# Optimization experiments

Measured on AMD Instinct MI355X. Metric: run time of the kernel, lower is better.

The kernel has to match this reference:

```python
import jax, jax.numpy as jnp
import numpy as np

H = 32        # query heads
KVH = 8       # key/value heads
D = 64        # head_dim
HID = 2048
B, S = 2, 2048

def rotate_half(x):
    x1, x2 = x[..., :D // 2], x[..., D // 2:]
    return jnp.concatenate((-x2, x1), axis=-1)

def setup_inputs() -> dict:
    key = jax.random.key(0)
    ks = jax.random.split(key, 7)
    scale = 1.0 / np.sqrt(HID)
    return {
        "x": jax.random.normal(ks[0], (B, S, HID), jnp.float32),
        "cos": jax.random.uniform(ks[1], (S, D), jnp.float32),
        "sin": jax.random.uniform(ks[2], (S, D), jnp.float32),
        "wq": jax.random.normal(ks[3], (HID, H * D), jnp.float32) * scale,
        "wk": jax.random.normal(ks[4], (HID, KVH * D), jnp.float32) * scale,
        "wv": jax.random.normal(ks[5], (HID, KVH * D), jnp.float32) * scale,
        "wo": jax.random.normal(ks[6], (HID, HID), jnp.float32) * scale,
    }

def reference(x, cos, sin, wq, wk, wv, wo):
    b, s, _ = x.shape
    # QKV projections -> [b, heads, s, d]
    q = (x @ wq).reshape(b, s, H, D).transpose(0, 2, 1, 3)
    k = (x @ wk).reshape(b, s, KVH, D).transpose(0, 2, 1, 3)
    v = (x @ wv).reshape(b, s, KVH, D).transpose(0, 2, 1, 3)
    # RoPE (cos/sin broadcast over batch and heads)
    c = cos[None, None, :, :]
    si = sin[None, None, :, :]
    q = q * c + rotate_half(q) * si
    k = k * c + rotate_half(k) * si
    # GQA: expand kv heads (repeat_interleave on head axis)
    g = H // KVH
    k = jnp.repeat(k, g, axis=1)
    v = jnp.repeat(v, g, axis=1)
    # causal SDPA
    scores = jnp.einsum("bhqd,bhkd->bhqk", q, k) / np.sqrt(D).astype(np.float32)
    causal = jnp.tril(jnp.ones((s, s), dtype=bool))
    scores = jnp.where(causal[None, None], scores, jnp.finfo(scores.dtype).min)
    attn = jax.nn.softmax(scores, axis=-1)
    out = jnp.einsum("bhqk,bhkd->bhqd", attn, v)
    out = out.transpose(0, 2, 1, 3).reshape(b, s, H * D)
    return out @ wo
```

## Files before the change

kernel.cpp:

```cpp
#include <hip/hip_runtime.h>
#include <stdint.h>

#define B_ 2
#define S_ 2048
#define H_ 32
#define KVH_ 8
#define D_ 64
#define HID_ 2048

typedef float f32x4 __attribute__((ext_vector_type(4)));
typedef float f32x16 __attribute__((ext_vector_type(16)));
typedef short bf16x8 __attribute__((ext_vector_type(8)));
typedef unsigned short u16;
typedef unsigned short u16x4 __attribute__((ext_vector_type(4)));
typedef unsigned short u16x8 __attribute__((ext_vector_type(8)));
typedef unsigned int u32;
typedef unsigned int u32x2 __attribute__((ext_vector_type(2)));
typedef unsigned int u32x4 __attribute__((ext_vector_type(4)));

__device__ __forceinline__ u16 f2b(float f) {
  unsigned u = __builtin_bit_cast(unsigned, f);
  u += 0x7fffu + ((u >> 16) & 1u);
  return (u16)(u >> 16);
}
__device__ __forceinline__ float b2f(u16 h) {
  unsigned u = ((unsigned)h) << 16;
  return __builtin_bit_cast(float, u);
}
__device__ __forceinline__ void gl_lds16(const void* g, void* l) {
  __builtin_amdgcn_global_load_lds(
      (const __attribute__((address_space(1))) unsigned*)g,
      (__attribute__((address_space(3))) unsigned*)l, 16, 0, 0);
}
__device__ __forceinline__ f32x4 mfma16(bf16x8 a, bf16x8 b, f32x4 c) {
  return __builtin_amdgcn_mfma_f32_16x16x32_bf16(a, b, c, 0, 0, 0);
}
__device__ __forceinline__ f32x16 mfma32(bf16x8 a, bf16x8 b, f32x16 c) {
  return __builtin_amdgcn_mfma_f32_32x32x16_bf16(a, b, c, 0, 0, 0);
}
__device__ __forceinline__ u32 cvtpk(float lo, float hi) {
  u32 r;
  asm("v_cvt_pk_bf16_f32 %0, %1, %2" : "=v"(r) : "v"(lo), "v"(hi));
  return r;
}
__device__ __forceinline__ float fast_exp2(float x) {
#if __has_builtin(__builtin_amdgcn_exp2f)
  return __builtin_amdgcn_exp2f(x);
#else
  return exp2f(x);
#endif
}
__device__ __forceinline__ void swap32(u32 a, u32 b, u32& x, u32& y) {
#if __has_builtin(__builtin_amdgcn_permlane32_swap)
  auto r = __builtin_amdgcn_permlane32_swap(a, b, false, false);
  x = r[0];
  y = r[1];
#else
  u32 sa = (u32)__shfl_xor((int)a, 32), sb = (u32)__shfl_xor((int)b, 32);
  bool hib = (threadIdx.x & 32) != 0;
  x = hib ? sb : a;
  y = hib ? b : sa;
#endif
}

__global__ __launch_bounds__(256) void k_prep(const float* __restrict__ x,
                                              u16* __restrict__ xb,
                                              const float* __restrict__ wq,
                                              const float* __restrict__ wk,
                                              const float* __restrict__ wv,
                                              const float* __restrict__ wo,
                                              u16* __restrict__ wqkvT,
                                              u16* __restrict__ woT) {
  __shared__ float t[32][33];
  int bx = blockIdx.x;
  if (bx < 8192) {
    int i = bx * 256 + threadIdx.x;
    f32x4 v = *(const f32x4*)(x + (size_t)i * 4);
    u16x4 o;
    o[0] = f2b(v[0]); o[1] = f2b(v[1]); o[2] = f2b(v[2]); o[3] = f2b(v[3]);
    *(u16x4*)(xb + (size_t)i * 4) = o;
    return;
  }
  int tt2 = bx - 8192;
  int bxx = tt2 % 160;
  int ky = tt2 / 160;
  const int K = 2048;
  const float* src;
  u16* dst;
  int N, n0;
  if (bxx < 64) {
    src = wq; dst = wqkvT; N = 2048; n0 = bxx * 32;
  } else if (bxx < 80) {
    src = wk; dst = wqkvT + (size_t)2048 * 2048; N = 512; n0 = (bxx - 64) * 32;
  } else if (bxx < 96) {
    src = wv; dst = wqkvT + (size_t)2560 * 2048; N = 512; n0 = (bxx - 80) * 32;
  } else {
    src = wo; dst = woT; N = 2048; n0 = (bxx - 96) * 32;
  }
  int k0 = ky * 32;
  int tt = threadIdx.x;
  int r = tt >> 3, c4 = (tt & 7) << 2;
  f32x4 v = *(const f32x4*)(src + (size_t)(k0 + r) * N + n0 + c4);
  t[r][c4 + 0] = v[0]; t[r][c4 + 1] = v[1];
  t[r][c4 + 2] = v[2]; t[r][c4 + 3] = v[3];
  __syncthreads();
  u16x4 o;
  o[0] = f2b(t[c4 + 0][r]); o[1] = f2b(t[c4 + 1][r]);
  o[2] = f2b(t[c4 + 2][r]); o[3] = f2b(t[c4 + 3][r]);
  *(u16x4*)(dst + (size_t)(n0 + r) * K + k0 + c4) = o;
}

__device__ __forceinline__ void stage64(const u16* __restrict__ G, int rowbase,
                                        int K, int kt, u16* unit, int tid) {
  int r = tid >> 3, sl = tid & 7;
  gl_lds16(G + (size_t)(rowbase + r) * K + kt * 64 + ((sl ^ (r & 7)) << 3),
           (char*)unit + tid * 16);
}

template <int BN, int OUTF32>
__global__ __launch_bounds__(512, 1) void k_gemm8(const u16* __restrict__ A,
                                                  const u16* __restrict__ BT,
                                                  float* __restrict__ Cf,
                                                  u16* __restrict__ Cb,
                                                  int M, int N, int K) {
  constexpr int ATILE = 256 * 64;
  constexpr int BTILE = BN * 64;
  constexpr int BU = BN / 64;
  constexpr int WN = (BN == 128) ? 2 : 4;
  constexpr int NI = (BN == 192) ? 3 : 4;
  constexpr int MI = (BN == 128) ? 4 : 8;
  constexpr int MIP = MI / 4;
  __shared__ __align__(16) u16 sm[2 * ATILE + 2 * BTILE];
  const int tid = threadIdx.x;
  const int l = tid & 63;
  const int lg = (l >> 4) & 3, lr = l & 15;
  const int w = tid >> 6;
  const int wm = w / WN, wn = w % WN;

  const int nwg = gridDim.x;
  const int cpx = nwg >> 3;
  const int bid = blockIdx.x;
  const int swz = (bid & 7) * cpx + (bid >> 3);
  const int ntn = N / BN;
  const int bm = swz / ntn, bn = swz % ntn;
  const int m0 = bm << 8, n0 = bn * BN;

  const u16* Ag = A + (size_t)m0 * K;
  const u16* Bg = BT + (size_t)n0 * K;
  u16* As = sm;
  u16* Bs = sm + 2 * ATILE;

  const int nt = K >> 6;
  f32x4 acc[MI][NI] = {};

#pragma unroll
  for (int u = 0; u < 4; ++u) stage64(Ag, u * 64, K, 0, As + u * 4096, tid);
#pragma unroll
  for (int u = 0; u < BU; ++u) stage64(Bg, u * 64, K, 0, Bs + u * 4096, tid);
  stage64(Ag, 0, K, 1, As + ATILE, tid);
  stage64(Ag, 64, K, 1, As + ATILE + 4096, tid);
  asm volatile("s_waitcnt vmcnt(2)" ::: "memory");
  __builtin_amdgcn_s_barrier();
  asm volatile("" ::: "memory");

  for (int t = 0; t < nt; ++t) {
    const int cur = t & 1;
    u16* Ac = As + cur * ATILE;
    u16* Bc = Bs + cur * BTILE;
    u16* An = As + (cur ^ 1) * ATILE;
    u16* Bn = Bs + (cur ^ 1) * BTILE;
    bf16x8 bc[NI][2];
#pragma unroll
    for (int q = 0; q < 4; ++q) {
      bf16x8 af[MIP][2];
#pragma unroll
      for (int mi2 = 0; mi2 < MIP; ++mi2)
#pragma unroll
        for (int ks = 0; ks < 2; ++ks) {
          int row = wm * (MI * 16) + (q * MIP + mi2) * 16 + lr;
          int slot = (ks * 4 + lg) ^ (lr & 7);
          af[mi2][ks] = *(const bf16x8*)&Ac[row * 64 + slot * 8];
        }
      if (q == 0) {
#pragma unroll
        for (int ni = 0; ni < NI; ++ni)
#pragma unroll
          for (int ks = 0; ks < 2; ++ks) {
            int row = wn * (NI * 16) + ni * 16 + lr;
            int slot = (ks * 4 + lg) ^ (lr & 7);
            bc[ni][ks] = *(const bf16x8*)&Bc[row * 64 + slot * 8];
          }
      }
      if (t + 1 < nt) {
        if (q == 0) {
          stage64(Ag, 128, K, t + 1, An + 2 * 4096, tid);
          stage64(Ag, 192, K, t + 1, An + 3 * 4096, tid);
        } else if (q == 1) {
          stage64(Bg, 0, K, t + 1, Bn, tid);
          stage64(Bg, 64, K, t + 1, Bn + 4096, tid);
        } else if (q == 2) {
          if (BU >= 3) stage64(Bg, 128, K, t + 1, Bn + 2 * 4096, tid);
          if (BU >= 4) stage64(Bg, 192, K, t + 1, Bn + 3 * 4096, tid);
        }
      }
      __builtin_amdgcn_s_barrier();
      asm volatile("" ::: "memory");
      __builtin_amdgcn_s_setprio(1);
#pragma unroll
      for (int mi2 = 0; mi2 < MIP; ++mi2)
#pragma unroll
        for (int ni = 0; ni < NI; ++ni)
#pragma unroll
          for (int ks = 0; ks < 2; ++ks)
            acc[q * MIP + mi2][ni] =
                mfma16(af[mi2][ks], bc[ni][ks], acc[q * MIP + mi2][ni]);
      __builtin_amdgcn_s_setprio(0);
      if (q == 3) {
        if (t + 2 < nt) {
          stage64(Ag, 0, K, t + 2, Ac, tid);
          stage64(Ag, 64, K, t + 2, Ac + 4096, tid);
          asm volatile("s_waitcnt vmcnt(2)" ::: "memory");
        } else if (t + 1 < nt) {
          asm volatile("s_waitcnt vmcnt(0)" ::: "memory");
        }
      }
      __builtin_amdgcn_s_barrier();
      asm volatile("" ::: "memory");
    }
  }

#pragma unroll
  for (int mi = 0; mi < MI; ++mi)
#pragma unroll
    for (int ni = 0; ni < NI; ++ni)
#pragma unroll
      for (int j = 0; j < 4; ++j) {
        size_t row = (size_t)m0 + wm * (MI * 16) + mi * 16 + lg * 4 + j;
        size_t col = (size_t)n0 + wn * (NI * 16) + ni * 16 + lr;
        if (OUTF32)
          Cf[row * N + col] = acc[mi][ni][j];
        else
          Cb[row * N + col] = f2b(acc[mi][ni][j]);
      }
}

__global__ __launch_bounds__(256) void k_ropev(const u16* __restrict__ qkv,
                                               const float* __restrict__ cosb,
                                               const float* __restrict__ sinb,
                                               u16* __restrict__ Kr,
                                               u16* __restrict__ Vt) {
  __shared__ u16 t[64][72];
  int bx = blockIdx.x;
  if (bx < 2048) {
    int task = bx * 16 + (threadIdx.x >> 4);
    int t16 = threadIdx.x & 15;
    int kvh = task & 7;
    int row = task >> 3;
    int b = row >> 11, s = row & (S_ - 1);
    int d2 = t16 * 2;
    const u16* base = qkv + (size_t)row * 3072 + 2048 + kvh * 64;
    u32 lo = *(const u32*)(base + d2);
    u32 hi = *(const u32*)(base + d2 + 32);
    float xl0 = b2f((u16)lo), xl1 = b2f((u16)(lo >> 16));
    float xh0 = b2f((u16)hi), xh1 = b2f((u16)(hi >> 16));
    const float* cb = cosb + s * 64;
    const float* sb = sinb + s * 64;
    float cl0 = cb[d2], cl1 = cb[d2 + 1], ch0 = cb[d2 + 32], ch1 = cb[d2 + 33];
    float sl0 = sb[d2], sl1 = sb[d2 + 1], sh0 = sb[d2 + 32], sh1 = sb[d2 + 33];
    float ol0 = xl0 * cl0 - xh0 * sl0;
    float ol1 = xl1 * cl1 - xh1 * sl1;
    float oh0 = xh0 * ch0 + xl0 * sh0;
    float oh1 = xh1 * ch1 + xl1 * sh1;
    u16* dst = Kr + ((size_t)(b * KVH_ + kvh) * S_ + s) * 64;
    *(u32*)(dst + d2) = (u32)f2b(ol0) | ((u32)f2b(ol1) << 16);
    *(u32*)(dst + d2 + 32) = (u32)f2b(oh0) | ((u32)f2b(oh1) << 16);
    return;
  }
  int bid = bx - 2048;
  int st = bid & 31, kvh = (bid >> 5) & 7, b = bid >> 8;
  int s0 = st * 64;
  int tid = threadIdx.x;
  int sl = tid >> 2, c16 = (tid & 3) << 4;
  const u16* src = qkv + (size_t)(b * S_ + s0 + sl) * 3072 + 2560 + kvh * 64 + c16;
  u16x8 v0 = *(const u16x8*)src;
  u16x8 v1 = *(const u16x8*)(src + 8);
#pragma unroll
  for (int i = 0; i < 8; ++i) { t[sl][c16 + i] = v0[i]; t[sl][c16 + 8 + i] = v1[i]; }
  __syncthreads();
  int dl = tid >> 2, s16 = (tid & 3) << 4;
  u16x8 o0, o1;
#pragma unroll
  for (int i = 0; i < 8; ++i) { o0[i] = t[s16 + i][dl]; o1[i] = t[s16 + 8 + i][dl]; }
  u16* dst = Vt + ((size_t)(b * KVH_ + kvh) * 64 + dl) * S_ + s0 + s16;
  *(u16x8*)dst = o0;
  *(u16x8*)(dst + 8) = o1;
}

__device__ __forceinline__ void stage_kv8(const u16* __restrict__ Kg,
                                          const u16* __restrict__ Vg, int k0,
                                          u16* ldsK, u16* ldsV, int tid) {
  int r = tid >> 3, cc = tid & 7;
  gl_lds16(Kg + (size_t)(k0 + r) * 64 + ((cc ^ (r & 7)) << 3), ldsK + tid * 8);
  gl_lds16(Vg + (size_t)r * S_ + k0 + ((cc ^ (r & 7)) << 3), ldsV + tid * 8);
}

__device__ __forceinline__ void repack2(const f32x16 s, bf16x8& f0, bf16x8& f1) {
  bf16x8 outv[2];
#pragma unroll
  for (int h = 0; h < 2; ++h) {
    u32 a0 = cvtpk(s[8 * h + 0], s[8 * h + 1]);
    u32 a1 = cvtpk(s[8 * h + 4], s[8 * h + 5]);
    u32 b0 = cvtpk(s[8 * h + 2], s[8 * h + 3]);
    u32 b1 = cvtpk(s[8 * h + 6], s[8 * h + 7]);
    u32 x0, y0, x1, y1;
    swap32(a0, a1, x0, y0);
    swap32(b0, b1, x1, y1);
    u32x4 t;
    t[0] = x0; t[1] = x1; t[2] = y0; t[3] = y1;
    outv[h] = __builtin_bit_cast(bf16x8, t);
  }
  f0 = outv[0];
  f1 = outv[1];
}

__global__ __launch_bounds__(512) void k_attn(const u16* __restrict__ qkv,
                                              const u16* __restrict__ Kr,
                                              const u16* __restrict__ Vt,
                                              const float* __restrict__ cosb,
                                              const float* __restrict__ sinb,
                                              u16* __restrict__ Oout) {
  __shared__ __align__(16) u16 lds[16384];
  const int tid = threadIdx.x;
  const int w = tid >> 6, l = tid & 63;
  const int hi = l >> 5, l31 = l & 31;

  const int bid = blockIdx.x;
  const int g = bid >> 6;
  const int qtl = (g < 4) ? (7 - g) : (g - 4);
  const int hh = (bid >> 1) & 31;
  const int b = bid & 1;
  const int kvh = hh >> 2;
  const int q0 = qtl * 256;
  const int qw0 = q0 + w * 32;
  const int nt = 4 * qtl + 4;

  int off8[4];
#pragma unroll
  for (int c = 0; c < 4; ++c)
    off8[c] = l31 * 64 + ((((c << 1) | hi) ^ (l31 & 7)) << 3);

  const int s_q = qw0 + l31;
  const u16* qsrc = qkv + (size_t)(b * S_ + s_q) * 3072 + hh * 64;
  bf16x8 qf[4];
  {
    const float* cb = cosb + s_q * 64;
    const float* sb = sinb + s_q * 64;
#pragma unroll
    for (int cp = 0; cp < 2; ++cp) {
      bf16x8 rlo = *(const bf16x8*)(qsrc + cp * 16 + hi * 8);
      bf16x8 rhi = *(const bf16x8*)(qsrc + 32 + cp * 16 + hi * 8);
      int dlo = cp * 16 + hi * 8;
      float ol[8], oh[8];
#pragma unroll
      for (int j = 0; j < 8; ++j) {
        float ql = b2f((u16)rlo[j]), qh = b2f((u16)rhi[j]);
        ol[j] = (ql * cb[dlo + j] - qh * sb[dlo + j]) * 0.18033688f;
        oh[j] = (qh * cb[dlo + 32 + j] + ql * sb[dlo + 32 + j]) * 0.18033688f;
      }
      u32x4 plo, phi;
#pragma unroll
      for (int j2 = 0; j2 < 4; ++j2) {
        plo[j2] = cvtpk(ol[2 * j2], ol[2 * j2 + 1]);
        phi[j2] = cvtpk(oh[2 * j2], oh[2 * j2 + 1]);
      }
      qf[cp] = __builtin_bit_cast(bf16x8, plo);
      qf[cp + 2] = __builtin_bit_cast(bf16x8, phi);
    }
  }

  const u16* Kg = Kr + (size_t)(b * KVH_ + kvh) * S_ * 64;
  const u16* Vg = Vt + (size_t)(b * KVH_ + kvh) * 64 * S_;

  f32x16 o0 = {}, o1 = {};
  float l_run = 0.f;

  stage_kv8(Kg, Vg, 0, lds, lds + 4096, tid);
  asm volatile("s_waitcnt vmcnt(0)" ::: "memory");
  __builtin_amdgcn_s_barrier();
  asm volatile("" ::: "memory");

  for (int kt = 0; kt < nt; ++kt) {
    const int cur = kt & 1;
    const int k0 = kt * 64;
    if (kt + 1 < nt)
      stage_kv8(Kg, Vg, k0 + 64, lds + (cur ^ 1) * 8192,
                lds + (cur ^ 1) * 8192 + 4096, tid);

    if (k0 <= qw0 + 31) {
      const u16* Kc = lds + cur * 8192;
      const u16* Vc = Kc + 4096;

      f32x16 sl = {}, sh = {};
      __builtin_amdgcn_s_setprio(1);
#pragma unroll
      for (int c = 0; c < 4; ++c) {
        bf16x8 klo = *(const bf16x8*)(Kc + off8[c]);
        bf16x8 khi = *(const bf16x8*)(Kc + 2048 + off8[c]);
        sl = mfma32(klo, qf[c], sl);
        sh = mfma32(khi, qf[c], sh);
      }
      __builtin_amdgcn_s_setprio(0);

      if (k0 + 63 > qw0) {
        int qg = qw0 + l31;
#pragma unroll
        for (int r = 0; r < 16; ++r) {
          int kg = k0 + (r & 3) + 8 * (r >> 2) + 4 * hi;
          if (kg > qg) sl[r] = -3e38f;
          if (kg + 32 > qg) sh[r] = -3e38f;
        }
      }

      float smv[16];
#pragma unroll
      for (int i = 0; i < 16; ++i) {
        sl[i] = fast_exp2(sl[i]);
        sh[i] = fast_exp2(sh[i]);
        smv[i] = sl[i] + sh[i];
      }
#pragma unroll
      for (int i = 0; i < 8; ++i) smv[i] += smv[i + 8];
#pragma unroll
      for (int i = 0; i < 4; ++i) smv[i] += smv[i + 4];
      smv[0] = (smv[0] + smv[2]) + (smv[1] + smv[3]);
      l_run += smv[0] + __shfl_xor(smv[0], 32);

      bf16x8 pf[4];
      repack2(sl, pf[0], pf[1]);
      repack2(sh, pf[2], pf[3]);

      __builtin_amdgcn_s_setprio(1);
#pragma unroll
      for (int sub = 0; sub < 4; ++sub) {
        bf16x8 v0 = *(const bf16x8*)(Vc + off8[sub]);
        bf16x8 v1 = *(const bf16x8*)(Vc + 2048 + off8[sub]);
        o0 = mfma32(v0, pf[sub], o0);
        o1 = mfma32(v1, pf[sub], o1);
      }
      __builtin_amdgcn_s_setprio(0);
    }

    asm volatile("s_waitcnt vmcnt(0)" ::: "memory");
    __builtin_amdgcn_s_barrier();
    asm volatile("" ::: "memory");
  }

  {
    u16* ep = lds + w * 2048;
    float inv = 1.0f / l_run;
    float oc[32];
#pragma unroll
    for (int i = 0; i < 16; ++i) { oc[i] = o0[i]; oc[16 + i] = o1[i]; }
#pragma unroll
    for (int dh = 0; dh < 2; ++dh)
#pragma unroll
      for (int g2 = 0; g2 < 4; ++g2) {
        u32 w0 = cvtpk(oc[dh * 16 + 4 * g2 + 0] * inv, oc[dh * 16 + 4 * g2 + 1] * inv);
        u32 w1 = cvtpk(oc[dh * 16 + 4 * g2 + 2] * inv, oc[dh * 16 + 4 * g2 + 3] * inv);
        int col = dh * 32 + 8 * g2 + 4 * hi;
        u32x2 tw; tw[0] = w0; tw[1] = w1;
        *(u32x2*)&ep[l31 * 64 + col] = tw;
      }
    asm volatile("s_waitcnt lgkmcnt(0)" ::: "memory");
    int row = l >> 1;
    size_t gb = ((size_t)(b * S_ + q0 + w * 32 + row)) * HID_ + hh * 64 + (l & 1) * 32;
#pragma unroll
    for (int cc = 0; cc < 4; ++cc) {
      u16x8 v = *(const u16x8*)&ep[row * 64 + (l & 1) * 32 + cc * 8];
      *(u16x8*)&Oout[gb + cc * 8] = v;
    }
  }
}

extern "C" void kernel_launch(void* const* d_in, const int* in_sizes, int n_in,
                              void* d_out, int out_size, void* d_ws, size_t ws_size,
                              hipStream_t stream) {
  (void)in_sizes; (void)n_in; (void)out_size; (void)ws_size;
  const float* x    = (const float*)d_in[0];
  const float* cosb = (const float*)d_in[1];
  const float* sinb = (const float*)d_in[2];
  const float* wq   = (const float*)d_in[3];
  const float* wk   = (const float*)d_in[4];
  const float* wv   = (const float*)d_in[5];
  const float* wo   = (const float*)d_in[6];

  char* wsb = (char*)d_ws;
  u16* xb    = (u16*)(wsb + 0);
  u16* wqkvT = (u16*)(wsb + 16777216);
  u16* woT   = (u16*)(wsb + 29360128);
  u16* qkv   = (u16*)(wsb + 37748736);
  u16* attno = (u16*)(wsb + 62914560);
  u16* Kr    = (u16*)(wsb + 79691776);
  u16* Vt    = (u16*)(wsb + 83886080);

  k_prep<<<18432, 256, 0, stream>>>(x, xb, wq, wk, wv, wo, wqkvT, woT);

  k_gemm8<192, 0><<<256, 512, 0, stream>>>(xb, wqkvT, nullptr, qkv, 4096, 3072, 2048);

  k_ropev<<<2560, 256, 0, stream>>>(qkv, cosb, sinb, Kr, Vt);

  k_attn<<<512, 512, 0, stream>>>(qkv, Kr, Vt, cosb, sinb, attno);

  k_gemm8<128, 1><<<256, 512, 0, stream>>>(attno, woT, (float*)d_out, nullptr,
                                           4096, 2048, 2048);
}
```

Measured before the change: 172.3 us.

## Double GEMM workgroup to 16 waves with half acting as loaders

Both GEMM launches go from 512 to 1024 threads per workgroup. The 256xBN tile is now split across 16 waves, each computing a 64-row by BN/4-column subtile, and only the first 8 waves issue the global-to-LDS staging loads. The aim is more waves per CU to hide LDS and MFMA latency, with fewer accumulators per wave so register pressure drops. In exchange, each wave reloads B fragments, so per-wave LDS traffic rises relative to its MFMA work, and barriers now synchronise twice as many waves.

Result: no change. 172.9 us (+0.4%).

```diff
diff --git a/kernel.cpp b/kernel.cpp
--- a/kernel.cpp
+++ b/kernel.cpp
@@ -118,24 +118,25 @@
 }
 
 template <int BN, int OUTF32>
-__global__ __launch_bounds__(512, 1) void k_gemm8(const u16* __restrict__ A,
-                                                  const u16* __restrict__ BT,
-                                                  float* __restrict__ Cf,
-                                                  u16* __restrict__ Cb,
-                                                  int M, int N, int K) {
+__global__ __launch_bounds__(1024, 1) void k_gemm8(const u16* __restrict__ A,
+                                                   const u16* __restrict__ BT,
+                                                   float* __restrict__ Cf,
+                                                   u16* __restrict__ Cb,
+                                                   int M, int N, int K) {
   constexpr int ATILE = 256 * 64;
   constexpr int BTILE = BN * 64;
   constexpr int BU = BN / 64;
-  constexpr int WN = (BN == 128) ? 2 : 4;
-  constexpr int NI = (BN == 192) ? 3 : 4;
-  constexpr int MI = (BN == 128) ? 4 : 8;
-  constexpr int MIP = MI / 4;
+  constexpr int WN = 4;
+  constexpr int NI = BN / 64;
+  constexpr int MI = 4;
   __shared__ __align__(16) u16 sm[2 * ATILE + 2 * BTILE];
   const int tid = threadIdx.x;
   const int l = tid & 63;
   const int lg = (l >> 4) & 3, lr = l & 15;
   const int w = tid >> 6;
-  const int wm = w / WN, wn = w % WN;
+  const int wm = w >> 2, wn = w & 3;
+  const bool stager = (w < 8);
+  const int stid = tid & 511;
 
   const int nwg = gridDim.x;
   const int cpx = nwg >> 3;
@@ -153,13 +154,15 @@
   const int nt = K >> 6;
   f32x4 acc[MI][NI] = {};
 
-#pragma unroll
-  for (int u = 0; u < 4; ++u) stage64(Ag, u * 64, K, 0, As + u * 4096, tid);
-#pragma unroll
-  for (int u = 0; u < BU; ++u) stage64(Bg, u * 64, K, 0, Bs + u * 4096, tid);
-  stage64(Ag, 0, K, 1, As + ATILE, tid);
-  stage64(Ag, 64, K, 1, As + ATILE + 4096, tid);
-  asm volatile("s_waitcnt vmcnt(2)" ::: "memory");
+  if (stager) {
+#pragma unroll
+    for (int u = 0; u < 4; ++u) stage64(Ag, u * 64, K, 0, As + u * 4096, stid);
+#pragma unroll
+    for (int u = 0; u < BU; ++u) stage64(Bg, u * 64, K, 0, Bs + u * 4096, stid);
+    stage64(Ag, 0, K, 1, As + ATILE, stid);
+    stage64(Ag, 64, K, 1, As + ATILE + 4096, stid);
+    asm volatile("s_waitcnt vmcnt(2)" ::: "memory");
+  }
   __builtin_amdgcn_s_barrier();
   asm volatile("" ::: "memory");
 
@@ -172,15 +175,13 @@
     bf16x8 bc[NI][2];
 #pragma unroll
     for (int q = 0; q < 4; ++q) {
-      bf16x8 af[MIP][2];
-#pragma unroll
-      for (int mi2 = 0; mi2 < MIP; ++mi2)
-#pragma unroll
-        for (int ks = 0; ks < 2; ++ks) {
-          int row = wm * (MI * 16) + (q * MIP + mi2) * 16 + lr;
-          int slot = (ks * 4 + lg) ^ (lr & 7);
-          af[mi2][ks] = *(const bf16x8*)&Ac[row * 64 + slot * 8];
-        }
+      bf16x8 af[2];
+#pragma unroll
+      for (int ks = 0; ks < 2; ++ks) {
+        int row = wm * 64 + q * 16 + lr;
+        int slot = (ks * 4 + lg) ^ (lr & 7);
+        af[ks] = *(const bf16x8*)&Ac[row * 64 + slot * 8];
+      }
       if (q == 0) {
 #pragma unroll
         for (int ni = 0; ni < NI; ++ni)
@@ -191,37 +192,36 @@
             bc[ni][ks] = *(const bf16x8*)&Bc[row * 64 + slot * 8];
           }
       }
-      if (t + 1 < nt) {
+      if (stager && t + 1 < nt) {
         if (q == 0) {
-          stage64(Ag, 128, K, t + 1, An + 2 * 4096, tid);
-          stage64(Ag, 192, K, t + 1, An + 3 * 4096, tid);
+          stage64(Ag, 128, K, t + 1, An + 2 * 4096, stid);
+          stage64(Ag, 192, K, t + 1, An + 3 * 4096, stid);
         } else if (q == 1) {
-          stage64(Bg, 0, K, t + 1, Bn, tid);
-          stage64(Bg, 64, K, t + 1, Bn + 4096, tid);
+          stage64(Bg, 0, K, t + 1, Bn, stid);
+          stage64(Bg, 64, K, t + 1, Bn + 4096, stid);
         } else if (q == 2) {
-          if (BU >= 3) stage64(Bg, 128, K, t + 1, Bn + 2 * 4096, tid);
-          if (BU >= 4) stage64(Bg, 192, K, t + 1, Bn + 3 * 4096, tid);
+          if (BU >= 3) stage64(Bg, 128, K, t + 1, Bn + 2 * 4096, stid);
+          if (BU >= 4) stage64(Bg, 192, K, t + 1, Bn + 3 * 4096, stid);
         }
       }
       __builtin_amdgcn_s_barrier();
       asm volatile("" ::: "memory");
       __builtin_amdgcn_s_setprio(1);
 #pragma unroll
-      for (int mi2 = 0; mi2 < MIP; ++mi2)
-#pragma unroll
-        for (int ni = 0; ni < NI; ++ni)
-#pragma unroll
-          for (int ks = 0; ks < 2; ++ks)
-            acc[q * MIP + mi2][ni] =
-                mfma16(af[mi2][ks], bc[ni][ks], acc[q * MIP + mi2][ni]);
+      for (int ni = 0; ni < NI; ++ni)
+#pragma unroll
+        for (int ks = 0; ks < 2; ++ks)
+          acc[q][ni] = mfma16(af[ks], bc[ni][ks], acc[q][ni]);
       __builtin_amdgcn_s_setprio(0);
       if (q == 3) {
-        if (t + 2 < nt) {
-          stage64(Ag, 0, K, t + 2, Ac, tid);
-          stage64(Ag, 64, K, t + 2, Ac + 4096, tid);
-          asm volatile("s_waitcnt vmcnt(2)" ::: "memory");
-        } else if (t + 1 < nt) {
-          asm volatile("s_waitcnt vmcnt(0)" ::: "memory");
+        if (stager) {
+          if (t + 2 < nt) {
+            stage64(Ag, 0, K, t + 2, Ac, stid);
+            stage64(Ag, 64, K, t + 2, Ac + 4096, stid);
+            asm volatile("s_waitcnt vmcnt(2)" ::: "memory");
+          } else if (t + 1 < nt) {
+            asm volatile("s_waitcnt vmcnt(0)" ::: "memory");
+          }
         }
       }
       __builtin_amdgcn_s_barrier();
@@ -235,7 +235,7 @@
     for (int ni = 0; ni < NI; ++ni)
 #pragma unroll
       for (int j = 0; j < 4; ++j) {
-        size_t row = (size_t)m0 + wm * (MI * 16) + mi * 16 + lg * 4 + j;
+        size_t row = (size_t)m0 + wm * 64 + mi * 16 + lg * 4 + j;
         size_t col = (size_t)n0 + wn * (NI * 16) + ni * 16 + lr;
         if (OUTF32)
           Cf[row * N + col] = acc[mi][ni][j];
@@ -505,12 +505,12 @@
 
   k_prep<<<18432, 256, 0, stream>>>(x, xb, wq, wk, wv, wo, wqkvT, woT);
 
-  k_gemm8<192, 0><<<256, 512, 0, stream>>>(xb, wqkvT, nullptr, qkv, 4096, 3072, 2048);
+  k_gemm8<192, 0><<<256, 1024, 0, stream>>>(xb, wqkvT, nullptr, qkv, 4096, 3072, 2048);
 
   k_ropev<<<2560, 256, 0, stream>>>(qkv, cosb, sinb, Kr, Vt);
 
   k_attn<<<512, 512, 0, stream>>>(qkv, Kr, Vt, cosb, sinb, attno);
 
-  k_gemm8<128, 1><<<256, 512, 0, stream>>>(attno, woT, (float*)d_out, nullptr,
-                                           4096, 2048, 2048);
-}
+  k_gemm8<128, 1><<<256, 1024, 0, stream>>>(attno, woT, (float*)d_out, nullptr,
+                                            4096, 2048, 2048);
+}
```
